# Optimization experiments

Measured on AMD Instinct MI355X. Metric: run time of the kernel, lower is better.

## Reference

```python
import jax, jax.numpy as jnp
import numpy as np

B, L, W, H = 16, 256, 4, 128
N = L + W - 1  # 259
EPS = 1e-6


def setup_inputs() -> dict:
    key = jax.random.key(0)
    k1, k2 = jax.random.split(key)
    x1 = jax.random.normal(k1, (B, 1, N, H), dtype=jnp.float32)
    x2 = jax.random.normal(k2, (B, 1, N, H), dtype=jnp.float32)
    return {"x1": x1, "x2": x2}


def _attention_matrix(x1, x2):
    # x1: (B,1,n,d); x2.permute(0,2,1,3): (B,n,1,d) -> broadcast diff (B,n,n,d)
    diff = x1 - jnp.transpose(x2, (0, 2, 1, 3))
    euclid = jnp.sqrt(jnp.sum(diff * diff, axis=3) + EPS)  # (B,n,n)
    return 1.0 / (euclid + 1.0)


def _wp(x, a):
    # x: (B,1,n,H), a: (B,n) -> weighted sliding-window sum over W positions
    wx = x * a[:, None, :, None]  # (B,1,n,H)
    out = wx[:, :, 0:L, :]
    for k in range(1, W):  # small fixed loop over filter width
        out = out + wx[:, :, k:k + L, :]
    return out  # (B,1,L,H)


def reference(x1, x2):
    att = _attention_matrix(x1, x2)      # (B,n,n)
    x1_a = jnp.sum(att, axis=1)          # (B,n) weight per x1 position
    x2_a = jnp.sum(att, axis=2)          # (B,n) weight per x2 position
    return (_wp(x1, x1_a), _wp(x2, x2_a))
```

## Files before the change

kernel.cpp:

```cpp
#include <hip/hip_runtime.h>
#include <hip/hip_bf16.h>
#include <math.h>

#define Bn  16
#define Ln  256
#define Wn  4
#define Hn  128
#define Nn  259
#define EPSF 1e-6f
#define PSTR 320
#define X2AP_OFF (5 * Bn * PSTR)

typedef float f32x4 __attribute__((ext_vector_type(4)));
typedef short s16x8 __attribute__((ext_vector_type(8)));

__device__ float g_part[2 * X2AP_OFF];

__device__ __forceinline__ unsigned short bfb(float x) {
    union { __hip_bfloat16 h; unsigned short u; } t;
    t.h = __float2bfloat16(x);
    return t.u;
}

__global__ __launch_bounds__(256) void att2(const float* __restrict__ x1,
                                            const float* __restrict__ x2) {
    __shared__ unsigned short As[64 * 136];
    __shared__ unsigned short Bs[64 * 136];
    __shared__ float n2s[64], n1s[64];
    __shared__ float colpart[4 * 64];

    const int it = blockIdx.x, jt = blockIdx.y, b = blockIdx.z;
    const int i0 = it * 64, j0 = jt * 64;
    const int tid = threadIdx.x;

    const float* __restrict__ x1b = x1 + (size_t)b * Nn * Hn;
    const float* __restrict__ x2b = x2 + (size_t)b * Nn * Hn;

    #pragma unroll
    for (int iter = 0; iter < 8; ++iter) {
        const int idx = iter * 256 + tid;
        const int r = idx >> 5, c4 = idx & 31;
        float4 va = make_float4(0.f, 0.f, 0.f, 0.f), vb = va;
        if (i0 + r < Nn) va = ((const float4*)(x2b + (i0 + r) * Hn))[c4];
        if (j0 + r < Nn) vb = ((const float4*)(x1b + (j0 + r) * Hn))[c4];
        const unsigned long long pa =
            (unsigned long long)bfb(va.x)        | ((unsigned long long)bfb(va.y) << 16) |
            ((unsigned long long)bfb(va.z) << 32) | ((unsigned long long)bfb(va.w) << 48);
        const unsigned long long pb =
            (unsigned long long)bfb(vb.x)        | ((unsigned long long)bfb(vb.y) << 16) |
            ((unsigned long long)bfb(vb.z) << 32) | ((unsigned long long)bfb(vb.w) << 48);
        *((unsigned long long*)&As[r * 136 + c4 * 4]) = pa;
        *((unsigned long long*)&Bs[r * 136 + c4 * 4]) = pb;
    }
    __syncthreads();

    const int w = tid >> 6, lane = tid & 63;
    const int rsel = lane & 15, q = lane >> 4;

    f32x4 acc[4] = {{0,0,0,0}, {0,0,0,0}, {0,0,0,0}, {0,0,0,0}};
    f32x4 accA = {0,0,0,0}, accB = {0,0,0,0};
    const unsigned short* arow  = &As[(w * 16 + rsel) * 136 + q * 8];
    const unsigned short* bnrow = &Bs[(w * 16 + rsel) * 136 + q * 8];
    const unsigned short* brow  = &Bs[rsel * 136 + q * 8];
    #pragma unroll
    for (int s = 0; s < 4; ++s) {
        const s16x8 af = *((const s16x8*)(arow + s * 32));
        const s16x8 bn = *((const s16x8*)(bnrow + s * 32));
        accA = __builtin_amdgcn_mfma_f32_16x16x32_bf16(af, af, accA, 0, 0, 0);
        accB = __builtin_amdgcn_mfma_f32_16x16x32_bf16(bn, bn, accB, 0, 0, 0);
        #pragma unroll
        for (int t = 0; t < 4; ++t) {
            const s16x8 bf = *((const s16x8*)(brow + t * 16 * 136 + s * 32));
            acc[t] = __builtin_amdgcn_mfma_f32_16x16x32_bf16(af, bf, acc[t], 0, 0, 0);
        }
    }

    if (q == (rsel >> 2)) {
        n2s[w * 16 + rsel] = accA[rsel & 3];
        n1s[w * 16 + rsel] = accB[rsel & 3];
    }
    __syncthreads();

    float rowacc[4] = {0.f, 0.f, 0.f, 0.f};
    #pragma unroll
    for (int t = 0; t < 4; ++t) {
        const int   j   = j0 + t * 16 + rsel;
        const bool  jv  = (j < Nn);
        const float n1v = n1s[t * 16 + rsel];
        float cp = 0.f;
        #pragma unroll
        for (int reg = 0; reg < 4; ++reg) {
            const int   i   = i0 + w * 16 + q * 4 + reg;
            const float e   = fmaf(-2.f, acc[t][reg], n2s[w * 16 + q * 4 + reg] + n1v + EPSF);
            const float att = ((i < Nn) && jv)
                ? __builtin_amdgcn_rcpf(__builtin_amdgcn_sqrtf(e) + 1.f) : 0.f;
            rowacc[reg] += att;
            cp          += att;
        }
        cp += __shfl_xor(cp, 16);
        cp += __shfl_xor(cp, 32);
        if (q == 0) colpart[w * 64 + t * 16 + rsel] = cp;
    }
    #pragma unroll
    for (int reg = 0; reg < 4; ++reg) {
        float rs = rowacc[reg];
        #pragma unroll
        for (int off = 8; off; off >>= 1) rs += __shfl_down(rs, off, 16);
        const int i = i0 + w * 16 + q * 4 + reg;
        if (rsel == 0 && i < Nn)
            g_part[X2AP_OFF + (jt * Bn + b) * PSTR + i] = rs;
    }
    __syncthreads();
    if (tid < 64) {
        const int j = j0 + tid;
        if (j < Nn)
            g_part[(it * Bn + b) * PSTR + j] =
                colpart[tid] + colpart[64 + tid] + colpart[128 + tid] + colpart[192 + tid];
    }
}

__global__ __launch_bounds__(256) void wp_kernel(const float* __restrict__ x1,
                                                 const float* __restrict__ x2,
                                                 float* __restrict__ out) {
    __shared__ float a_s[11];
    const int PER = Bn * Ln * Hn / 4;
    const int blk = blockIdx.x;
    const bool second = blk >= 512;
    const int eb = (second ? blk - 512 : blk) * 256;
    const int b  = eb >> 13;
    const int l0 = (eb & 8191) >> 5;

    const float* x = second ? x2 : x1;
    const float* p = g_part + (second ? X2AP_OFF : 0) + b * PSTR;
    if (threadIdx.x < 11) {
        const int j = l0 + threadIdx.x;
        float s = 0.f;
        #pragma unroll
        for (int t = 0; t < 5; ++t) s += p[t * (Bn * PSTR) + j];
        a_s[threadIdx.x] = s;
    }
    __syncthreads();

    const int e  = eb + threadIdx.x;
    const int l  = (e & 8191) >> 5;
    const int h4 = e & 31;
    const float4* xb = (const float4*)(x + (size_t)b * Nn * Hn);
    float4 acc = make_float4(0.f, 0.f, 0.f, 0.f);
    #pragma unroll
    for (int k = 0; k < Wn; ++k) {
        const float  av = a_s[l - l0 + k];
        const float4 xv = xb[(l + k) * (Hn / 4) + h4];
        acc.x += av * xv.x;
        acc.y += av * xv.y;
        acc.z += av * xv.z;
        acc.w += av * xv.w;
    }
    ((float4*)out)[(second ? PER : 0) + e] = acc;
}

extern "C" void kernel_launch(void* const* d_in, const int* in_sizes, int n_in,
                              void* d_out, int out_size, void* d_ws, size_t ws_size,
                              hipStream_t stream) {
    const float* x1 = (const float*)d_in[0];
    const float* x2 = (const float*)d_in[1];
    (void)d_ws; (void)ws_size;

    dim3 gridA(5, 5, Bn);
    att2<<<gridA, 256, 0, stream>>>(x1, x2);

    wp_kernel<<<1024, 256, 0, stream>>>(x1, x2, (float*)d_out);
}
```

Baseline: 68.86 us.

## Fuse attention and window-sum kernels with a grid-wide atomic barrier

Merges the attention-partial kernel and the weighted window-sum kernel into one launch. A software grid barrier (atomic counter plus spin with s_sleep) makes all 400 blocks finish writing partial sums before they loop over the 1024 output tiles. This removes one kernel launch and the gap between kernels. In exchange it depends on all 400 blocks being resident at once to avoid deadlock, and it adds barrier spin cost.

```diff
diff --git a/kernel.cpp b/kernel.cpp
--- a/kernel.cpp
+++ b/kernel.cpp
@@ -10,11 +10,13 @@
 #define EPSF 1e-6f
 #define PSTR 320
 #define X2AP_OFF (5 * Bn * PSTR)
+#define NBLK 400
 
 typedef float f32x4 __attribute__((ext_vector_type(4)));
 typedef short s16x8 __attribute__((ext_vector_type(8)));
 
 __device__ float g_part[2 * X2AP_OFF];
+__device__ int g_bar;
 
 __device__ __forceinline__ unsigned short bfb(float x) {
     union { __hip_bfloat16 h; unsigned short u; } t;
@@ -22,12 +24,14 @@
     return t.u;
 }
 
-__global__ __launch_bounds__(256) void att2(const float* __restrict__ x1,
-                                            const float* __restrict__ x2) {
+__global__ __launch_bounds__(256, 2) void fused(const float* __restrict__ x1,
+                                                const float* __restrict__ x2,
+                                                float* __restrict__ out) {
     __shared__ unsigned short As[64 * 136];
     __shared__ unsigned short Bs[64 * 136];
     __shared__ float n2s[64], n1s[64];
     __shared__ float colpart[4 * 64];
+    __shared__ float a_s[11];
 
     const int it = blockIdx.x, jt = blockIdx.y, b = blockIdx.z;
     const int i0 = it * 64, j0 = jt * 64;
@@ -117,45 +121,57 @@
             g_part[(it * Bn + b) * PSTR + j] =
                 colpart[tid] + colpart[64 + tid] + colpart[128 + tid] + colpart[192 + tid];
     }
-}
 
-__global__ __launch_bounds__(256) void wp_kernel(const float* __restrict__ x1,
-                                                 const float* __restrict__ x2,
-                                                 float* __restrict__ out) {
-    __shared__ float a_s[11];
-    const int PER = Bn * Ln * Hn / 4;
-    const int blk = blockIdx.x;
-    const bool second = blk >= 512;
-    const int eb = (second ? blk - 512 : blk) * 256;
-    const int b  = eb >> 13;
-    const int l0 = (eb & 8191) >> 5;
-
-    const float* x = second ? x2 : x1;
-    const float* p = g_part + (second ? X2AP_OFF : 0) + b * PSTR;
-    if (threadIdx.x < 11) {
-        const int j = l0 + threadIdx.x;
-        float s = 0.f;
-        #pragma unroll
-        for (int t = 0; t < 5; ++t) s += p[t * (Bn * PSTR) + j];
-        a_s[threadIdx.x] = s;
+    __threadfence();
+    __syncthreads();
+    if (tid == 0) {
+        const int t = __hip_atomic_fetch_add(&g_bar, 1, __ATOMIC_ACQ_REL,
+                                             __HIP_MEMORY_SCOPE_AGENT);
+        const int target = (t / NBLK) * NBLK + NBLK;
+        while (__hip_atomic_load(&g_bar, __ATOMIC_ACQUIRE,
+                                 __HIP_MEMORY_SCOPE_AGENT) < target) {
+            __builtin_amdgcn_s_sleep(2);
+        }
     }
     __syncthreads();
+    __threadfence();
 
-    const int e  = eb + threadIdx.x;
-    const int l  = (e & 8191) >> 5;
-    const int h4 = e & 31;
-    const float4* xb = (const float4*)(x + (size_t)b * Nn * Hn);
-    float4 acc = make_float4(0.f, 0.f, 0.f, 0.f);
-    #pragma unroll
-    for (int k = 0; k < Wn; ++k) {
-        const float  av = a_s[l - l0 + k];
-        const float4 xv = xb[(l + k) * (Hn / 4) + h4];
-        acc.x += av * xv.x;
-        acc.y += av * xv.y;
-        acc.z += av * xv.z;
-        acc.w += av * xv.w;
+    const int lin = blockIdx.x + 5 * blockIdx.y + 25 * blockIdx.z;
+    const int PER = Bn * Ln * Hn / 4;
+    for (int blk = lin; blk < 1024; blk += NBLK) {
+        __syncthreads();
+        const bool second = blk >= 512;
+        const int eb = (second ? blk - 512 : blk) * 256;
+        const int cb  = eb >> 13;
+        const int l0 = (eb & 8191) >> 5;
+
+        const float* x = second ? x2 : x1;
+        const float* p = g_part + (second ? X2AP_OFF : 0) + cb * PSTR;
+        if (tid < 11) {
+            const int j = l0 + tid;
+            float s = 0.f;
+            #pragma unroll
+            for (int t = 0; t < 5; ++t) s += p[t * (Bn * PSTR) + j];
+            a_s[tid] = s;
+        }
+        __syncthreads();
+
+        const int e  = eb + tid;
+        const int l  = (e & 8191) >> 5;
+        const int h4 = e & 31;
+        const float4* xb = (const float4*)(x + (size_t)cb * Nn * Hn);
+        float4 accw = make_float4(0.f, 0.f, 0.f, 0.f);
+        #pragma unroll
+        for (int k = 0; k < Wn; ++k) {
+            const float  av = a_s[l - l0 + k];
+            const float4 xv = xb[(l + k) * (Hn / 4) + h4];
+            accw.x += av * xv.x;
+            accw.y += av * xv.y;
+            accw.z += av * xv.z;
+            accw.w += av * xv.w;
+        }
+        ((float4*)out)[(second ? PER : 0) + e] = accw;
     }
-    ((float4*)out)[(second ? PER : 0) + e] = acc;
 }
 
 extern "C" void kernel_launch(void* const* d_in, const int* in_sizes, int n_in,
@@ -166,7 +182,5 @@
     (void)d_ws; (void)ws_size;
 
     dim3 gridA(5, 5, Bn);
-    att2<<<gridA, 256, 0, stream>>>(x1, x2);
-
-    wp_kernel<<<1024, 256, 0, stream>>>(x1, x2, (float*)d_out);
+    fused<<<gridA, 256, 0, stream>>>(x1, x2, (float*)d_out);
 }
```

New measurement: 168.0 us. +144.0%, slower.

## Precompute bf16 inputs and norms, fuse attention row sums into windowed-product kernel

Applied to the files above, without the earlier changes.

Adds a conversion kernel that writes bf16 copies of x1 and x2 plus per-row squared norms into global scratch. The attention tiles are no longer computed in a separate pass; each windowed-product block now computes, with MFMA, the 11 attention row sums it needs against all key rows and then applies the weighted sliding window. This removes the partial-sum scratch round trip and the conversion work that every tile repeated, but each block recomputes distances for overlapping rows (11 of every 16 computed), so redundant MFMA work is spread across 1024 blocks.

```diff
diff --git a/kernel.cpp b/kernel.cpp
--- a/kernel.cpp
+++ b/kernel.cpp
@@ -7,155 +7,123 @@
 #define Wn  4
 #define Hn  128
 #define Nn  259
+#define NPAD 320
 #define EPSF 1e-6f
-#define PSTR 320
-#define X2AP_OFF (5 * Bn * PSTR)
 
 typedef float f32x4 __attribute__((ext_vector_type(4)));
 typedef short s16x8 __attribute__((ext_vector_type(8)));
 
-__device__ float g_part[2 * X2AP_OFF];
+__device__ unsigned short g_c[2][Bn][NPAD][Hn];
+__device__ float          g_nrm[2][Bn][NPAD];
 
 __device__ __forceinline__ unsigned short bfb(float x) {
     union { __hip_bfloat16 h; unsigned short u; } t;
     t.h = __float2bfloat16(x);
     return t.u;
 }
-
-__global__ __launch_bounds__(256) void att2(const float* __restrict__ x1,
-                                            const float* __restrict__ x2) {
-    __shared__ unsigned short As[64 * 136];
-    __shared__ unsigned short Bs[64 * 136];
-    __shared__ float n2s[64], n1s[64];
-    __shared__ float colpart[4 * 64];
-
-    const int it = blockIdx.x, jt = blockIdx.y, b = blockIdx.z;
-    const int i0 = it * 64, j0 = jt * 64;
-    const int tid = threadIdx.x;
-
-    const float* __restrict__ x1b = x1 + (size_t)b * Nn * Hn;
-    const float* __restrict__ x2b = x2 + (size_t)b * Nn * Hn;
-
-    #pragma unroll
-    for (int iter = 0; iter < 8; ++iter) {
-        const int idx = iter * 256 + tid;
-        const int r = idx >> 5, c4 = idx & 31;
-        float4 va = make_float4(0.f, 0.f, 0.f, 0.f), vb = va;
-        if (i0 + r < Nn) va = ((const float4*)(x2b + (i0 + r) * Hn))[c4];
-        if (j0 + r < Nn) vb = ((const float4*)(x1b + (j0 + r) * Hn))[c4];
-        const unsigned long long pa =
-            (unsigned long long)bfb(va.x)        | ((unsigned long long)bfb(va.y) << 16) |
-            ((unsigned long long)bfb(va.z) << 32) | ((unsigned long long)bfb(va.w) << 48);
-        const unsigned long long pb =
-            (unsigned long long)bfb(vb.x)        | ((unsigned long long)bfb(vb.y) << 16) |
-            ((unsigned long long)bfb(vb.z) << 32) | ((unsigned long long)bfb(vb.w) << 48);
-        *((unsigned long long*)&As[r * 136 + c4 * 4]) = pa;
-        *((unsigned long long*)&Bs[r * 136 + c4 * 4]) = pb;
-    }
-    __syncthreads();
-
-    const int w = tid >> 6, lane = tid & 63;
-    const int rsel = lane & 15, q = lane >> 4;
-
-    f32x4 acc[4] = {{0,0,0,0}, {0,0,0,0}, {0,0,0,0}, {0,0,0,0}};
-    f32x4 accA = {0,0,0,0}, accB = {0,0,0,0};
-    const unsigned short* arow  = &As[(w * 16 + rsel) * 136 + q * 8];
-    const unsigned short* bnrow = &Bs[(w * 16 + rsel) * 136 + q * 8];
-    const unsigned short* brow  = &Bs[rsel * 136 + q * 8];
-    #pragma unroll
-    for (int s = 0; s < 4; ++s) {
-        const s16x8 af = *((const s16x8*)(arow + s * 32));
-        const s16x8 bn = *((const s16x8*)(bnrow + s * 32));
-        accA = __builtin_amdgcn_mfma_f32_16x16x32_bf16(af, af, accA, 0, 0, 0);
-        accB = __builtin_amdgcn_mfma_f32_16x16x32_bf16(bn, bn, accB, 0, 0, 0);
-        #pragma unroll
-        for (int t = 0; t < 4; ++t) {
-            const s16x8 bf = *((const s16x8*)(brow + t * 16 * 136 + s * 32));
-            acc[t] = __builtin_amdgcn_mfma_f32_16x16x32_bf16(af, bf, acc[t], 0, 0, 0);
-        }
-    }
-
-    if (q == (rsel >> 2)) {
-        n2s[w * 16 + rsel] = accA[rsel & 3];
-        n1s[w * 16 + rsel] = accB[rsel & 3];
-    }
-    __syncthreads();
-
-    float rowacc[4] = {0.f, 0.f, 0.f, 0.f};
-    #pragma unroll
-    for (int t = 0; t < 4; ++t) {
-        const int   j   = j0 + t * 16 + rsel;
-        const bool  jv  = (j < Nn);
-        const float n1v = n1s[t * 16 + rsel];
-        float cp = 0.f;
-        #pragma unroll
-        for (int reg = 0; reg < 4; ++reg) {
-            const int   i   = i0 + w * 16 + q * 4 + reg;
-            const float e   = fmaf(-2.f, acc[t][reg], n2s[w * 16 + q * 4 + reg] + n1v + EPSF);
-            const float att = ((i < Nn) && jv)
-                ? __builtin_amdgcn_rcpf(__builtin_amdgcn_sqrtf(e) + 1.f) : 0.f;
-            rowacc[reg] += att;
-            cp          += att;
-        }
-        cp += __shfl_xor(cp, 16);
-        cp += __shfl_xor(cp, 32);
-        if (q == 0) colpart[w * 64 + t * 16 + rsel] = cp;
-    }
-    #pragma unroll
-    for (int reg = 0; reg < 4; ++reg) {
-        float rs = rowacc[reg];
-        #pragma unroll
-        for (int off = 8; off; off >>= 1) rs += __shfl_down(rs, off, 16);
-        const int i = i0 + w * 16 + q * 4 + reg;
-        if (rsel == 0 && i < Nn)
-            g_part[X2AP_OFF + (jt * Bn + b) * PSTR + i] = rs;
-    }
-    __syncthreads();
-    if (tid < 64) {
-        const int j = j0 + tid;
-        if (j < Nn)
-            g_part[(it * Bn + b) * PSTR + j] =
-                colpart[tid] + colpart[64 + tid] + colpart[128 + tid] + colpart[192 + tid];
-    }
+__device__ __forceinline__ float bf2f(unsigned short u) {
+    union { unsigned int i; float f; } t;
+    t.i = (unsigned int)u << 16;
+    return t.f;
 }
 
-__global__ __launch_bounds__(256) void wp_kernel(const float* __restrict__ x1,
-                                                 const float* __restrict__ x2,
-                                                 float* __restrict__ out) {
+__global__ __launch_bounds__(256) void conv(const float* __restrict__ x1,
+                                            const float* __restrict__ x2) {
+    const int arr = blockIdx.x, b = blockIdx.y;
+    const int row = blockIdx.z * 8 + (threadIdx.x >> 5);
+    const int c4  = threadIdx.x & 31;
+    const float* srcb = (arr ? x2 : x1) + (size_t)b * Nn * Hn;
+
+    float4 v = make_float4(0.f, 0.f, 0.f, 0.f);
+    if (row < Nn) v = ((const float4*)(srcb + row * Hn))[c4];
+
+    const unsigned short u0 = bfb(v.x), u1 = bfb(v.y), u2 = bfb(v.z), u3 = bfb(v.w);
+    *((unsigned long long*)&g_c[arr][b][row][c4 * 4]) =
+        (unsigned long long)u0        | ((unsigned long long)u1 << 16) |
+        ((unsigned long long)u2 << 32) | ((unsigned long long)u3 << 48);
+
+    const float r0 = bf2f(u0), r1 = bf2f(u1), r2 = bf2f(u2), r3 = bf2f(u3);
+    float ss = r0 * r0 + r1 * r1 + r2 * r2 + r3 * r3;
+    #pragma unroll
+    for (int off = 16; off; off >>= 1) ss += __shfl_down(ss, off, 32);
+    if (c4 == 0) g_nrm[arr][b][row] = ss;
+}
+
+__global__ __launch_bounds__(256) void attwp(const float* __restrict__ x1,
+                                             const float* __restrict__ x2,
+                                             float* __restrict__ out) {
+    __shared__ float nks[NPAD];
+    __shared__ float awave[4][16];
     __shared__ float a_s[11];
-    const int PER = Bn * Ln * Hn / 4;
+
     const int blk = blockIdx.x;
     const bool second = blk >= 512;
     const int eb = (second ? blk - 512 : blk) * 256;
     const int b  = eb >> 13;
     const int l0 = (eb & 8191) >> 5;
+    const int tid = threadIdx.x;
 
-    const float* x = second ? x2 : x1;
-    const float* p = g_part + (second ? X2AP_OFF : 0) + b * PSTR;
-    if (threadIdx.x < 11) {
-        const int j = l0 + threadIdx.x;
-        float s = 0.f;
-        #pragma unroll
-        for (int t = 0; t < 5; ++t) s += p[t * (Bn * PSTR) + j];
-        a_s[threadIdx.x] = s;
-    }
+    const unsigned short* qc = &g_c[second ? 1 : 0][b][0][0];
+    const unsigned short* kc = &g_c[second ? 0 : 1][b][0][0];
+    const float* nq = &g_nrm[second ? 1 : 0][b][0];
+    const float* nk = &g_nrm[second ? 0 : 1][b][0];
+
+    if (tid < NPAD / 4) ((f32x4*)nks)[tid] = ((const f32x4*)nk)[tid];
+
+    const int w = tid >> 6, lane = tid & 63;
+    const int rsel = lane & 15, q = lane >> 4;
+
+    const unsigned short* qrow = qc + (l0 + rsel) * Hn + q * 8;
+    const s16x8 bq0 = *((const s16x8*)(qrow));
+    const s16x8 bq1 = *((const s16x8*)(qrow + 32));
+    const s16x8 bq2 = *((const s16x8*)(qrow + 64));
+    const s16x8 bq3 = *((const s16x8*)(qrow + 96));
+    const float nqv = nq[l0 + rsel];
     __syncthreads();
 
-    const int e  = eb + threadIdx.x;
+    float psum = 0.f;
+    const unsigned short* krow = kc + rsel * Hn + q * 8;
+    for (int tile = w; tile < 17; tile += 4) {
+        const unsigned short* kr = krow + tile * 16 * Hn;
+        f32x4 acc = {0, 0, 0, 0};
+        acc = __builtin_amdgcn_mfma_f32_16x16x32_bf16(*((const s16x8*)(kr)),      bq0, acc, 0, 0, 0);
+        acc = __builtin_amdgcn_mfma_f32_16x16x32_bf16(*((const s16x8*)(kr + 32)), bq1, acc, 0, 0, 0);
+        acc = __builtin_amdgcn_mfma_f32_16x16x32_bf16(*((const s16x8*)(kr + 64)), bq2, acc, 0, 0, 0);
+        acc = __builtin_amdgcn_mfma_f32_16x16x32_bf16(*((const s16x8*)(kr + 96)), bq3, acc, 0, 0, 0);
+        const int ibase = tile * 16 + q * 4;
+        const f32x4 nkv = *((const f32x4*)&nks[ibase]);
+        #pragma unroll
+        for (int reg = 0; reg < 4; ++reg) {
+            const float e   = fmaf(-2.f, acc[reg], nkv[reg] + nqv + EPSF);
+            const float att = __builtin_amdgcn_rcpf(__builtin_amdgcn_sqrtf(e) + 1.f);
+            psum += (ibase + reg < Nn) ? att : 0.f;
+        }
+    }
+    psum += __shfl_xor(psum, 16);
+    psum += __shfl_xor(psum, 32);
+    if (lane < 16) awave[w][lane] = psum;
+    __syncthreads();
+    if (tid < 11)
+        a_s[tid] = awave[0][tid] + awave[1][tid] + awave[2][tid] + awave[3][tid];
+    __syncthreads();
+
+    const int PER = Bn * Ln * Hn / 4;
+    const float* x = second ? x2 : x1;
+    const int e  = eb + tid;
     const int l  = (e & 8191) >> 5;
     const int h4 = e & 31;
     const float4* xb = (const float4*)(x + (size_t)b * Nn * Hn);
-    float4 acc = make_float4(0.f, 0.f, 0.f, 0.f);
+    float4 accw = make_float4(0.f, 0.f, 0.f, 0.f);
     #pragma unroll
     for (int k = 0; k < Wn; ++k) {
         const float  av = a_s[l - l0 + k];
         const float4 xv = xb[(l + k) * (Hn / 4) + h4];
-        acc.x += av * xv.x;
-        acc.y += av * xv.y;
-        acc.z += av * xv.z;
-        acc.w += av * xv.w;
+        accw.x += av * xv.x;
+        accw.y += av * xv.y;
+        accw.z += av * xv.z;
+        accw.w += av * xv.w;
     }
-    ((float4*)out)[(second ? PER : 0) + e] = acc;
+    ((float4*)out)[(second ? PER : 0) + e] = accw;
 }
 
 extern "C" void kernel_launch(void* const* d_in, const int* in_sizes, int n_in,
@@ -165,8 +133,6 @@
     const float* x2 = (const float*)d_in[1];
     (void)d_ws; (void)ws_size;
 
-    dim3 gridA(5, 5, Bn);
-    att2<<<gridA, 256, 0, stream>>>(x1, x2);
-
-    wp_kernel<<<1024, 256, 0, stream>>>(x1, x2, (float*)d_out);
+    conv<<<dim3(2, Bn, NPAD / 8), 256, 0, stream>>>(x1, x2);
+    attwp<<<1024, 256, 0, stream>>>(x1, x2, (float*)d_out);
 }
```

After: 72.24 us. 4.9% more time.
